# Optimization experiments

Measured on AMD Instinct MI355X. Metric: run time of the kernel, lower is better.

## Reference

```python
import jax, jax.numpy as jnp
import numpy as np

B, N, T, D, H, ET, C = 64, 64, 60, 4, 64, 4, 16
E = N * (N - 1)


def _forward(data, rel_type, rel_rec, rel_send, clinical,
             msg_w1, msg_b1, msg_w2, msg_b2,
             clinh_w1, clinh_b1, clinh_w2, clinh_b2, clinh_w3, clinh_b3,
             clinm_w1, clinm_b1, clinm_w2, clinm_b2, clinm_w3, clinm_b3,
             in_r_w, in_r_b, in_z_w, in_z_b, in_n_w, in_n_b,
             hr_w, hr_b, hn_w, hn_b,
             out1_w, out1_b, out2_w, out2_b, out3_w, out3_b):
    def mlp3(x, w1, b1, w2, b2, w3, b3):
        h1 = jax.nn.relu(x @ w1 + b1)
        h2 = jax.nn.relu(h1 @ w2 + b2)
        return h2 @ w3 + b3

    Bn, Nn, Tn, Dn = data.shape
    ETn = msg_w1.shape[0]
    inputs = jnp.transpose(data, (0, 2, 1, 3))  # [B,T,N,D]
    # cond_hidden: initial hidden from clinical MLP
    hidden = mlp3(clinical, clinh_w1, clinh_b1, clinh_w2, clinh_b2, clinh_w3, clinh_b3).reshape(Bn, Nn, -1)
    # cond_msgs: per-node clinical message embedding (constant across steps)
    cln_msg = mlp3(clinical, clinm_w1, clinm_b1, clinm_w2, clinm_b2, clinm_w3, clinm_b3).reshape(Bn, Nn, -1)

    def step(carry, _):
        x, h = carry  # x: [B,N,D], h: [B,N,H]
        recv = jnp.einsum('ea,bah->beh', rel_rec, h)
        send = jnp.einsum('ea,bah->beh', rel_send, h)
        pre = jnp.concatenate([recv, send], axis=-1)  # [B,E,2H]
        # all edge-type message MLPs batched over type axis t
        m = jnp.tanh(jnp.einsum('bef,tfh->bteh', pre, msg_w1) + msg_b1[None, :, None, :])
        m = jnp.tanh(jnp.einsum('bteh,thg->bteg', m, msg_w2) + msg_b2[None, :, None, :])
        all_msgs = jnp.einsum('bteh,bet->beh', m, rel_type) / ETn  # weight by rel_type, norm = edge_types
        agg = jnp.einsum('ea,beh->bah', rel_rec, all_msgs) / Dn + cln_msg  # [B,N,H]
        hr_a = agg @ hr_w + hr_b
        r = jax.nn.sigmoid(x @ in_r_w + in_r_b + hr_a)
        # NOTE: original code uses self.hr (not self.hz) for the z gate; bug preserved.
        z = jax.nn.sigmoid(x @ in_z_w + in_z_b + hr_a)
        n = jnp.tanh(x @ in_n_w + in_n_b + r * (agg @ hn_w + hn_b))
        h_new = (1.0 - z) * n + z * h
        p = jax.nn.relu(h_new @ out1_w + out1_b)
        p = jax.nn.relu(p @ out2_w + out2_b)
        pred = x + (p @ out3_w + out3_b)
        return (pred, h_new), pred

    x0 = inputs[:, 0]
    _, preds = jax.lax.scan(step, (x0, hidden), None, length=Tn - 1)  # [T-1,B,N,D]
    pred_all = jnp.concatenate([x0[None], preds], axis=0)  # [T,B,N,D]
    return jnp.transpose(pred_all, (1, 2, 0, 3))  # [B,N,T,D]


def setup_inputs() -> dict:
    key = jax.random.key(0)
    ks = jax.random.split(key, 64)
    cnt = [0]

    def nk():
        cnt[0] += 1
        return ks[cnt[0]]

    def p(shape):
        fan = shape[-2] if len(shape) > 1 else shape[0]
        return jax.random.normal(nk(), shape, jnp.float32) / np.sqrt(fan)

    off = ~np.eye(N, dtype=bool)
    eye = np.eye(N, dtype=np.float32)
    rel_rec = jnp.asarray(eye[np.where(off)[0]])   # [E,N] one-hot receivers
    rel_send = jnp.asarray(eye[np.where(off)[1]])  # [E,N] one-hot senders

    inp = {
        'data': jax.random.normal(nk(), (B, N, T, D), jnp.float32),
        'rel_type': jax.nn.softmax(jax.random.normal(nk(), (B, E, ET), jnp.float32), axis=-1),
        'rel_rec': rel_rec,
        'rel_send': rel_send,
        'clinical': jax.random.normal(nk(), (B, C), jnp.float32),
        'msg_w1': p((ET, 2 * H, H)), 'msg_b1': p((ET, H)),
        'msg_w2': p((ET, H, H)), 'msg_b2': p((ET, H)),
        'clinh_w1': p((C, H)), 'clinh_b1': p((H,)),
        'clinh_w2': p((H, 2 * H)), 'clinh_b2': p((2 * H,)),
        'clinh_w3': p((2 * H, N * H)), 'clinh_b3': p((N * H,)),
        'clinm_w1': p((C, H)), 'clinm_b1': p((H,)),
        'clinm_w2': p((H, 2 * H)), 'clinm_b2': p((2 * H,)),
        'clinm_w3': p((2 * H, N * H)), 'clinm_b3': p((N * H,)),
        'in_r_w': p((D, H)), 'in_r_b': p((H,)),
        'in_z_w': p((D, H)), 'in_z_b': p((H,)),
        'in_n_w': p((D, H)), 'in_n_b': p((H,)),
        'hr_w': p((H, H)), 'hr_b': p((H,)),
        'hn_w': p((H, H)), 'hn_b': p((H,)),
        'out1_w': p((H, H)), 'out1_b': p((H,)),
        'out2_w': p((H, H)), 'out2_b': p((H,)),
        'out3_w': p((H, D)), 'out3_b': p((D,)),
    }
    return inp


def reference(data, rel_type, rel_rec, rel_send, clinical,
              msg_w1, msg_b1, msg_w2, msg_b2,
              clinh_w1, clinh_b1, clinh_w2, clinh_b2, clinh_w3, clinh_b3,
              clinm_w1, clinm_b1, clinm_w2, clinm_b2, clinm_w3, clinm_b3,
              in_r_w, in_r_b, in_z_w, in_z_b, in_n_w, in_n_b,
              hr_w, hr_b, hn_w, hn_b,
              out1_w, out1_b, out2_w, out2_b, out3_w, out3_b):
    return _forward(data, rel_type, rel_rec, rel_send, clinical,
                    msg_w1, msg_b1, msg_w2, msg_b2,
                    clinh_w1, clinh_b1, clinh_w2, clinh_b2, clinh_w3, clinh_b3,
                    clinm_w1, clinm_b1, clinm_w2, clinm_b2, clinm_w3, clinm_b3,
                    in_r_w, in_r_b, in_z_w, in_z_b, in_n_w, in_n_b,
                    hr_w, hr_b, hn_w, hn_b,
                    out1_w, out1_b, out2_w, out2_b, out3_w, out3_b)
```

## Files before the change

kernel.cpp:

```cpp
#include <hip/hip_runtime.h>

#define Bz 64
#define Nz 64
#define Tz 60
#define Dz 4
#define Hz 64
#define ETz 4
#define Ez 4032

typedef _Float16 f16x8 __attribute__((ext_vector_type(8)));
typedef float    f32x4 __attribute__((ext_vector_type(4)));
typedef unsigned int u32;
typedef u32      u32x4 __attribute__((ext_vector_type(4)));
typedef unsigned short u16;

__device__ __forceinline__ float ftanh(float x) {
    float e = __expf(2.0f * x);
    return 1.0f - 2.0f * __builtin_amdgcn_rcpf(e + 1.0f);
}
__device__ __forceinline__ float fsig(float x) {
    return __builtin_amdgcn_rcpf(1.0f + __expf(-x));
}
__device__ __forceinline__ u32 pk2(_Float16 a, _Float16 b) {
    u32 ua = (u32)__builtin_bit_cast(u16, a);
    u32 ub = (u32)__builtin_bit_cast(u16, b);
    return ua | (ub << 16);
}

__global__ __launch_bounds__(64) void k_clinical(
    const float* __restrict__ clin,
    const float* __restrict__ hw1, const float* __restrict__ hb1,
    const float* __restrict__ hw2, const float* __restrict__ hb2,
    const float* __restrict__ hw3, const float* __restrict__ hb3,
    const float* __restrict__ mw1, const float* __restrict__ mb1,
    const float* __restrict__ mw2, const float* __restrict__ mb2,
    const float* __restrict__ mw3, const float* __restrict__ mb3,
    float* __restrict__ hidden, float* __restrict__ clnmsg)
{
    int bi = blockIdx.x;
    int b = bi >> 7, head = (bi >> 6) & 1, jb = bi & 63;
    int tid = threadIdx.x;
    const float* w1 = head ? mw1 : hw1; const float* b1 = head ? mb1 : hb1;
    const float* w2 = head ? mw2 : hw2; const float* b2v = head ? mb2 : hb2;
    const float* w3 = head ? mw3 : hw3; const float* b3 = head ? mb3 : hb3;
    float* outp = head ? clnmsg : hidden;

    __shared__ float sc[16], s1[64], s2[128];
    if (tid < 16) sc[tid] = clin[b * 16 + tid];
    __syncthreads();
    {
        float a = b1[tid];
        #pragma unroll
        for (int c = 0; c < 16; ++c) a = fmaf(sc[c], w1[c * 64 + tid], a);
        s1[tid] = fmaxf(a, 0.f);
    }
    __syncthreads();
    #pragma unroll
    for (int hh = 0; hh < 2; ++hh) {
        int jj = hh * 64 + tid;
        float a = b2v[jj];
        #pragma unroll 8
        for (int c = 0; c < 64; ++c) a = fmaf(s1[c], w2[c * 128 + jj], a);
        s2[jj] = fmaxf(a, 0.f);
    }
    __syncthreads();
    {
        int j = jb * 64 + tid;
        float a = b3[j];
        #pragma unroll 8
        for (int c = 0; c < 128; ++c) a = fmaf(s2[c], w3[c * 4096 + j], a);
        outp[b * 4096 + j] = a;
    }
}

__global__ __launch_bounds__(256) void k_wprep(const float* __restrict__ w2,
                                               u16* __restrict__ Whi,
                                               u16* __restrict__ Wlo)
{
    int id = blockIdx.x * 256 + threadIdx.x;
    int j = id & 7, L = (id >> 3) & 63, r = id >> 9;
    int kt = r & 1, n = (r >> 1) & 3, t = r >> 3;
    int k = kt * 32 + ((L >> 4) << 3) + j;
    int g = n * 16 + (L & 15);
    float w = w2[(t * 64 + k) * 64 + g];
    _Float16 h = (_Float16)w;
    _Float16 l = (_Float16)((w - (float)h) * 4096.0f);
    Whi[id] = __builtin_bit_cast(u16, h);
    Wlo[id] = __builtin_bit_cast(u16, l);
}

__global__ __launch_bounds__(256) void k_init(const float* __restrict__ data,
                                              float* __restrict__ xbuf,
                                              float* __restrict__ out)
{
    int i = blockIdx.x * 256 + threadIdx.x;
    int bn = i >> 2, d = i & 3;
    float v = data[bn * (Tz * Dz) + d];
    xbuf[i] = v;
    out[bn * (Tz * Dz) + d] = v;
}

__global__ __launch_bounds__(64) void k_proj2(
    const float* __restrict__ h, const float* __restrict__ w1,
    const float* __restrict__ b1,
    float* __restrict__ Hrb, float* __restrict__ Hs)
{
    int blk = blockIdx.x;
    int b = blk >> 5;
    int n0 = (blk & 31) * 2, n1 = n0 + 1;
    int l = threadIdx.x;
    __shared__ float s0[64], s1v[64];
    s0[l]  = h[(b * 64 + n0) * 64 + l];
    s1v[l] = h[(b * 64 + n1) * 64 + l];
    __syncthreads();
    #pragma unroll 1
    for (int t = 0; t < 4; ++t) {
        const float* w = w1 + t * 8192;
        float bb = b1[t * 64 + l];
        float ar0 = bb, as0 = 0.f, ar1 = bb, as1 = 0.f;
        #pragma unroll 8
        for (int c = 0; c < 64; ++c) {
            float wr = w[c * 64 + l];
            float wsv = w[(c + 64) * 64 + l];
            float h0 = s0[c], h1 = s1v[c];
            ar0 = fmaf(h0, wr, ar0); as0 = fmaf(h0, wsv, as0);
            ar1 = fmaf(h1, wr, ar1); as1 = fmaf(h1, wsv, as1);
        }
        Hrb[((b * 64 + n0) * 4 + t) * 64 + l] = ar0;
        Hrb[((b * 64 + n1) * 4 + t) * 64 + l] = ar1;
        Hs[((b * 4 + t) * 64 + l) * 64 + n0] = as0;
        Hs[((b * 4 + t) * 64 + l) * 64 + n1] = as1;
    }
}

__global__ __launch_bounds__(256, 5) void k_step(
    const float* __restrict__ Hrb, const float* __restrict__ Hs,
    const float* __restrict__ rel_type, const float* __restrict__ b2,
    const u16* __restrict__ Whi, const u16* __restrict__ Wlo,
    const float* __restrict__ cln,
    float* __restrict__ hbuf, float* __restrict__ xbuf,
    const float* __restrict__ irw, const float* __restrict__ irb,
    const float* __restrict__ izw, const float* __restrict__ izb,
    const float* __restrict__ inw, const float* __restrict__ inb,
    const float* __restrict__ hrw, const float* __restrict__ hrbv,
    const float* __restrict__ hnw, const float* __restrict__ hnbv,
    const float* __restrict__ o1w, const float* __restrict__ o1b,
    const float* __restrict__ o2w, const float* __restrict__ o2b,
    const float* __restrict__ o3w, const float* __restrict__ o3b,
    float* __restrict__ out, int tout)
{
    int blk = blockIdx.x;
    int b = blk >> 6, rv = blk & 63;
    int tid = threadIdx.x;
    int w = tid >> 6, L = tid & 63;
    int kg = L >> 4, el = L & 15;
    int e = w * 16 + el;

    __shared__ __align__(16) _Float16 ZaH[4][16][64];
    __shared__ __align__(16) _Float16 ZaL[4][16][64];
    __shared__ __align__(16) float srt[256];
    __shared__ float sRed[4][64];
    __shared__ float sA[64], sH[64], sP[64];

    {
        const float* rbase = rel_type + (b * Ez + rv * 63) * 4;
        float v = (tid < 252) ? rbase[tid] : 0.f;
        srt[(tid & 3) * 64 + (tid >> 2)] = v;
    }
    __syncthreads();

    int snd = (e < 63) ? (e + (e >= rv ? 1 : 0)) : 0;
    int em = el & 7;
    float pacc0 = 0.f, pacc1 = 0.f, pacc2 = 0.f, pacc3 = 0.f;

    #pragma unroll 1
    for (int t = 0; t < 4; ++t) {
        const float* hrp = Hrb + blk * 256 + t * 64 + kg * 16;
        const float* hsp = Hs + (b * 4 + t) * 4096 + kg * 1024 + snd;
        float zv[16];
        #pragma unroll
        for (int j = 0; j < 16; ++j) zv[j] = hrp[j] + hsp[j * 64];
        #pragma unroll
        for (int j = 0; j < 16; ++j) zv[j] = ftanh(zv[j]);

        #pragma unroll
        for (int p = 0; p < 2; ++p) {
            u32 hi[4], lo[4];
            #pragma unroll
            for (int q = 0; q < 4; ++q) {
                float a = zv[p * 8 + 2 * q], c = zv[p * 8 + 2 * q + 1];
                _Float16 ha = (_Float16)a, hc = (_Float16)c;
                _Float16 la = (_Float16)((a - (float)ha) * 4096.0f);
                _Float16 lc = (_Float16)((c - (float)hc) * 4096.0f);
                hi[q] = pk2(ha, hc);
                lo[q] = pk2(la, lc);
            }
            int cp = (2 * kg + p) ^ em;
            u32x4 vh = {hi[0], hi[1], hi[2], hi[3]};
            u32x4 vl = {lo[0], lo[1], lo[2], lo[3]};
            *(u32x4*)&ZaH[w][el][cp * 8] = vh;
            *(u32x4*)&ZaL[w][el][cp * 8] = vl;
        }

        f16x8 Ah[2], Al[2];
        #pragma unroll
        for (int kt = 0; kt < 2; ++kt) {
            int cp = (kt * 4 + kg) ^ em;
            Ah[kt] = *(const f16x8*)&ZaH[w][el][cp * 8];
            Al[kt] = *(const f16x8*)&ZaL[w][el][cp * 8];
        }

        f32x4 rt4 = *(const f32x4*)&srt[t * 64 + w * 16 + kg * 4];

        #pragma unroll
        for (int n = 0; n < 4; ++n) {
            const u16* wb = Whi + ((t * 8 + n * 2) * 64 + L) * 8;
            const u16* wl = Wlo + ((t * 8 + n * 2) * 64 + L) * 8;
            f16x8 Bh0 = *(const f16x8*)wb;
            f16x8 Bh1 = *(const f16x8*)(wb + 512);
            f16x8 Bl0 = *(const f16x8*)wl;
            f16x8 Bl1 = *(const f16x8*)(wl + 512);
            f32x4 hh = {0.f, 0.f, 0.f, 0.f};
            f32x4 cc = {0.f, 0.f, 0.f, 0.f};
            hh = __builtin_amdgcn_mfma_f32_16x16x32_f16(Ah[0], Bh0, hh, 0, 0, 0);
            hh = __builtin_amdgcn_mfma_f32_16x16x32_f16(Ah[1], Bh1, hh, 0, 0, 0);
            cc = __builtin_amdgcn_mfma_f32_16x16x32_f16(Ah[0], Bl0, cc, 0, 0, 0);
            cc = __builtin_amdgcn_mfma_f32_16x16x32_f16(Al[0], Bh0, cc, 0, 0, 0);
            cc = __builtin_amdgcn_mfma_f32_16x16x32_f16(Ah[1], Bl1, cc, 0, 0, 0);
            cc = __builtin_amdgcn_mfma_f32_16x16x32_f16(Al[1], Bh1, cc, 0, 0, 0);
            float b2n = b2[t * 64 + n * 16 + el];
            float acc = 0.f;
            #pragma unroll
            for (int r = 0; r < 4; ++r) {
                float v = fmaf(cc[r], (1.0f / 4096.0f), hh[r]) + b2n;
                acc = fmaf(ftanh(v), rt4[r], acc);
            }
            if (n == 0) pacc0 += acc;
            else if (n == 1) pacc1 += acc;
            else if (n == 2) pacc2 += acc;
            else pacc3 += acc;
        }
    }

    pacc0 += __shfl_xor(pacc0, 16); pacc0 += __shfl_xor(pacc0, 32);
    pacc1 += __shfl_xor(pacc1, 16); pacc1 += __shfl_xor(pacc1, 32);
    pacc2 += __shfl_xor(pacc2, 16); pacc2 += __shfl_xor(pacc2, 32);
    pacc3 += __shfl_xor(pacc3, 16); pacc3 += __shfl_xor(pacc3, 32);
    if (L < 16) {
        sRed[w][0 * 16 + L] = pacc0;
        sRed[w][1 * 16 + L] = pacc1;
        sRed[w][2 * 16 + L] = pacc2;
        sRed[w][3 * 16 + L] = pacc3;
    }
    __syncthreads();
    if (tid < 64) {
        float av = (sRed[0][tid] + sRed[1][tid] + sRed[2][tid] + sRed[3][tid]) * 0.0625f;
        sA[tid] = av + cln[blk * 64 + tid];
    }
    __syncthreads();

    if (w == 0) {
        float h_old = hbuf[blk * 64 + L];
        float x0 = xbuf[blk * 4 + 0], x1 = xbuf[blk * 4 + 1];
        float x2 = xbuf[blk * 4 + 2], x3 = xbuf[blk * 4 + 3];

        float hra = hrbv[L], hna = hnbv[L];
        #pragma unroll 8
        for (int k = 0; k < 64; ++k) {
            float av = sA[k];
            hra = fmaf(av, hrw[k * 64 + L], hra);
            hna = fmaf(av, hnw[k * 64 + L], hna);
        }
        float xr = irb[L], xz = izb[L], xn = inb[L];
        xr = fmaf(x0, irw[L], xr); xr = fmaf(x1, irw[64 + L], xr);
        xr = fmaf(x2, irw[128 + L], xr); xr = fmaf(x3, irw[192 + L], xr);
        xz = fmaf(x0, izw[L], xz); xz = fmaf(x1, izw[64 + L], xz);
        xz = fmaf(x2, izw[128 + L], xz); xz = fmaf(x3, izw[192 + L], xz);
        xn = fmaf(x0, inw[L], xn); xn = fmaf(x1, inw[64 + L], xn);
        xn = fmaf(x2, inw[128 + L], xn); xn = fmaf(x3, inw[192 + L], xn);

        float r = fsig(xr + hra);
        float z = fsig(xz + hra);
        float nn = ftanh(xn + r * hna);
        float hnew = (1.f - z) * nn + z * h_old;
        hbuf[blk * 64 + L] = hnew;
        sH[L] = hnew;

        float p = o1b[L];
        #pragma unroll 8
        for (int k = 0; k < 64; ++k) p = fmaf(sH[k], o1w[k * 64 + L], p);
        p = fmaxf(p, 0.f);
        sP[L] = p;
        float q = o2b[L];
        #pragma unroll 8
        for (int k = 0; k < 64; ++k) q = fmaf(sP[k], o2w[k * 64 + L], q);
        q = fmaxf(q, 0.f);
        sP[L] = q;
        if (L < 4) {
            float xv = (L == 0) ? x0 : (L == 1) ? x1 : (L == 2) ? x2 : x3;
            float pr = xv + o3b[L];
            #pragma unroll 8
            for (int k = 0; k < 64; ++k) pr = fmaf(sP[k], o3w[k * 4 + L], pr);
            out[(blk * Tz + tout) * 4 + L] = pr;
            xbuf[blk * 4 + L] = pr;
        }
    }
}

extern "C" void kernel_launch(void* const* d_in, const int* in_sizes, int n_in,
                              void* d_out, int out_size, void* d_ws, size_t ws_size,
                              hipStream_t stream)
{
    const float* data     = (const float*)d_in[0];
    const float* rel_type = (const float*)d_in[1];
    const float* clinical = (const float*)d_in[4];
    const float* msg_w1 = (const float*)d_in[5];
    const float* msg_b1 = (const float*)d_in[6];
    const float* msg_w2 = (const float*)d_in[7];
    const float* msg_b2 = (const float*)d_in[8];
    const float* chw1 = (const float*)d_in[9];
    const float* chb1 = (const float*)d_in[10];
    const float* chw2 = (const float*)d_in[11];
    const float* chb2 = (const float*)d_in[12];
    const float* chw3 = (const float*)d_in[13];
    const float* chb3 = (const float*)d_in[14];
    const float* cmw1 = (const float*)d_in[15];
    const float* cmb1 = (const float*)d_in[16];
    const float* cmw2 = (const float*)d_in[17];
    const float* cmb2 = (const float*)d_in[18];
    const float* cmw3 = (const float*)d_in[19];
    const float* cmb3 = (const float*)d_in[20];
    const float* irw = (const float*)d_in[21];
    const float* irb = (const float*)d_in[22];
    const float* izw = (const float*)d_in[23];
    const float* izb = (const float*)d_in[24];
    const float* inw = (const float*)d_in[25];
    const float* inb = (const float*)d_in[26];
    const float* hrw = (const float*)d_in[27];
    const float* hrb = (const float*)d_in[28];
    const float* hnw = (const float*)d_in[29];
    const float* hnb = (const float*)d_in[30];
    const float* o1w = (const float*)d_in[31];
    const float* o1b = (const float*)d_in[32];
    const float* o2w = (const float*)d_in[33];
    const float* o2b = (const float*)d_in[34];
    const float* o3w = (const float*)d_in[35];
    const float* o3b = (const float*)d_in[36];

    float* ws   = (float*)d_ws;
    float* hbuf = ws;
    float* cln  = ws + 262144;
    float* Hrb  = ws + 524288;
    float* Hs   = ws + 1572864;
    float* xbuf = ws + 2621440;
    u16*   Whi  = (u16*)(ws + 2637824);
    u16*   Wlo  = (u16*)(ws + 2646016);
    float* out  = (float*)d_out;

    k_clinical<<<dim3(8192), dim3(64), 0, stream>>>(
        clinical, chw1, chb1, chw2, chb2, chw3, chb3,
        cmw1, cmb1, cmw2, cmb2, cmw3, cmb3, hbuf, cln);
    k_wprep<<<dim3(64), dim3(256), 0, stream>>>(msg_w2, Whi, Wlo);
    k_init<<<dim3(64), dim3(256), 0, stream>>>(data, xbuf, out);
    k_proj2<<<dim3(2048), dim3(64), 0, stream>>>(hbuf, msg_w1, msg_b1, Hrb, Hs);

    for (int t = 1; t < Tz; ++t) {
        k_step<<<dim3(Bz * Nz), dim3(256), 0, stream>>>(
            Hrb, Hs, rel_type, msg_b2, Whi, Wlo, cln, hbuf, xbuf,
            irw, irb, izw, izb, inw, inb,
            hrw, hrb, hnw, hnb,
            o1w, o1b, o2w, o2b, o3w, o3b, out, t);
        if (t < Tz - 1)
            k_proj2<<<dim3(2048), dim3(64), 0, stream>>>(hbuf, msg_w1, msg_b1, Hrb, Hs);
    }
}
```

Before: 8.919 ms.

## Remap k_step warps to edge types and process two receiver nodes per block

Each warp now owns one edge type and keeps that type's hi/lo fp16 W2 fragments in registers. Each block handles two receiver nodes and loops over the edge tiles, where before each warp handled a tile of edges and reloaded weights for all four types. Hrb rows and rel_type are staged in shared memory for both nodes, and the grid is halved to 2048 blocks. The aim is to reuse weight loads across more edges, at the cost of higher register pressure (launch bounds lowered to 3) and fewer blocks.

Result: faster. 7.408 ms (-16.9%).

```diff
diff --git a/kernel.cpp b/kernel.cpp
--- a/kernel.cpp
+++ b/kernel.cpp
@@ -133,7 +133,68 @@
     }
 }
 
-__global__ __launch_bounds__(256, 5) void k_step(
+#define RV_TILES(RVS, PACC)                                                    \
+    {                                                                          \
+        const int rv = n0 + (RVS);                                             \
+        _Pragma("unroll 2")                                                    \
+        for (int m = 0; m < 4; ++m) {                                          \
+            int e = m * 16 + el;                                               \
+            int snd = (e < 63) ? (e + (e >= rv ? 1 : 0)) : 0;                  \
+            const float* hs = Hs + (b * 4 + w) * 4096 + kg * 1024 + snd;       \
+            float zv[16];                                                      \
+            _Pragma("unroll")                                                  \
+            for (int j = 0; j < 16; ++j)                                       \
+                zv[j] = sHr[(RVS) * 256 + w * 64 + kg * 16 + j] + hs[j * 64];  \
+            _Pragma("unroll")                                                  \
+            for (int j = 0; j < 16; ++j) zv[j] = ftanh(zv[j]);                 \
+            _Pragma("unroll")                                                  \
+            for (int p = 0; p < 2; ++p) {                                      \
+                u32 hi[4], lo[4];                                              \
+                _Pragma("unroll")                                              \
+                for (int q = 0; q < 4; ++q) {                                  \
+                    float a = zv[p * 8 + 2 * q], c = zv[p * 8 + 2 * q + 1];    \
+                    _Float16 ha = (_Float16)a, hc = (_Float16)c;               \
+                    _Float16 la = (_Float16)((a - (float)ha) * 4096.0f);       \
+                    _Float16 lc = (_Float16)((c - (float)hc) * 4096.0f);       \
+                    hi[q] = pk2(ha, hc);                                       \
+                    lo[q] = pk2(la, lc);                                       \
+                }                                                              \
+                int cp = (2 * kg + p) ^ em;                                    \
+                u32x4 vh = {hi[0], hi[1], hi[2], hi[3]};                       \
+                u32x4 vl = {lo[0], lo[1], lo[2], lo[3]};                       \
+                *(u32x4*)&ZaH[w][el][cp * 8] = vh;                             \
+                *(u32x4*)&ZaL[w][el][cp * 8] = vl;                             \
+            }                                                                  \
+            f16x8 Ah[2], Al[2];                                                \
+            _Pragma("unroll")                                                  \
+            for (int kt = 0; kt < 2; ++kt) {                                   \
+                int cp = (kt * 4 + kg) ^ em;                                   \
+                Ah[kt] = *(const f16x8*)&ZaH[w][el][cp * 8];                   \
+                Al[kt] = *(const f16x8*)&ZaL[w][el][cp * 8];                   \
+            }                                                                  \
+            f32x4 rt4 = *(const f32x4*)&srt[(RVS) * 256 + w * 64 + m * 16 + kg * 4]; \
+            _Pragma("unroll")                                                  \
+            for (int n = 0; n < 4; ++n) {                                      \
+                f32x4 hh = {0.f, 0.f, 0.f, 0.f};                               \
+                f32x4 cc = {0.f, 0.f, 0.f, 0.f};                               \
+                hh = __builtin_amdgcn_mfma_f32_16x16x32_f16(Ah[0], Bh[n*2+0], hh, 0, 0, 0); \
+                hh = __builtin_amdgcn_mfma_f32_16x16x32_f16(Ah[1], Bh[n*2+1], hh, 0, 0, 0); \
+                cc = __builtin_amdgcn_mfma_f32_16x16x32_f16(Ah[0], Bl[n*2+0], cc, 0, 0, 0); \
+                cc = __builtin_amdgcn_mfma_f32_16x16x32_f16(Al[0], Bh[n*2+0], cc, 0, 0, 0); \
+                cc = __builtin_amdgcn_mfma_f32_16x16x32_f16(Ah[1], Bl[n*2+1], cc, 0, 0, 0); \
+                cc = __builtin_amdgcn_mfma_f32_16x16x32_f16(Al[1], Bh[n*2+1], cc, 0, 0, 0); \
+                float acc = 0.f;                                               \
+                _Pragma("unroll")                                              \
+                for (int r = 0; r < 4; ++r) {                                  \
+                    float v = fmaf(cc[r], (1.0f / 4096.0f), hh[r]) + b2n[n];   \
+                    acc = fmaf(ftanh(v), rt4[r], acc);                         \
+                }                                                              \
+                PACC[n] += acc;                                                \
+            }                                                                  \
+        }                                                                      \
+    }
+
+__global__ __launch_bounds__(256, 3) void k_step(
     const float* __restrict__ Hrb, const float* __restrict__ Hs,
     const float* __restrict__ rel_type, const float* __restrict__ b2,
     const u16* __restrict__ Whi, const u16* __restrict__ Wlo,
@@ -150,124 +211,81 @@
     float* __restrict__ out, int tout)
 {
     int blk = blockIdx.x;
-    int b = blk >> 6, rv = blk & 63;
+    int b = blk >> 5;
+    int n0 = (blk & 31) * 2;
     int tid = threadIdx.x;
     int w = tid >> 6, L = tid & 63;
     int kg = L >> 4, el = L & 15;
-    int e = w * 16 + el;
+    int em = el & 7;
 
     __shared__ __align__(16) _Float16 ZaH[4][16][64];
     __shared__ __align__(16) _Float16 ZaL[4][16][64];
-    __shared__ __align__(16) float srt[256];
-    __shared__ float sRed[4][64];
-    __shared__ float sA[64], sH[64], sP[64];
-
-    {
-        const float* rbase = rel_type + (b * Ez + rv * 63) * 4;
-        float v = (tid < 252) ? rbase[tid] : 0.f;
-        srt[(tid & 3) * 64 + (tid >> 2)] = v;
-    }
-    __syncthreads();
-
-    int snd = (e < 63) ? (e + (e >= rv ? 1 : 0)) : 0;
-    int em = el & 7;
-    float pacc0 = 0.f, pacc1 = 0.f, pacc2 = 0.f, pacc3 = 0.f;
-
-    #pragma unroll 1
-    for (int t = 0; t < 4; ++t) {
-        const float* hrp = Hrb + blk * 256 + t * 64 + kg * 16;
-        const float* hsp = Hs + (b * 4 + t) * 4096 + kg * 1024 + snd;
-        float zv[16];
-        #pragma unroll
-        for (int j = 0; j < 16; ++j) zv[j] = hrp[j] + hsp[j * 64];
-        #pragma unroll
-        for (int j = 0; j < 16; ++j) zv[j] = ftanh(zv[j]);
-
-        #pragma unroll
-        for (int p = 0; p < 2; ++p) {
-            u32 hi[4], lo[4];
-            #pragma unroll
-            for (int q = 0; q < 4; ++q) {
-                float a = zv[p * 8 + 2 * q], c = zv[p * 8 + 2 * q + 1];
-                _Float16 ha = (_Float16)a, hc = (_Float16)c;
-                _Float16 la = (_Float16)((a - (float)ha) * 4096.0f);
-                _Float16 lc = (_Float16)((c - (float)hc) * 4096.0f);
-                hi[q] = pk2(ha, hc);
-                lo[q] = pk2(la, lc);
-            }
-            int cp = (2 * kg + p) ^ em;
-            u32x4 vh = {hi[0], hi[1], hi[2], hi[3]};
-            u32x4 vl = {lo[0], lo[1], lo[2], lo[3]};
-            *(u32x4*)&ZaH[w][el][cp * 8] = vh;
-            *(u32x4*)&ZaL[w][el][cp * 8] = vl;
-        }
-
-        f16x8 Ah[2], Al[2];
-        #pragma unroll
-        for (int kt = 0; kt < 2; ++kt) {
-            int cp = (kt * 4 + kg) ^ em;
-            Ah[kt] = *(const f16x8*)&ZaH[w][el][cp * 8];
-            Al[kt] = *(const f16x8*)&ZaL[w][el][cp * 8];
-        }
-
-        f32x4 rt4 = *(const f32x4*)&srt[t * 64 + w * 16 + kg * 4];
-
+    __shared__ __align__(16) float srt[512];
+    __shared__ __align__(16) float sHr[512];
+    __shared__ float sRed[4][2][64];
+    __shared__ float sA[128], sH[128], sP[128];
+
+    #pragma unroll
+    for (int it = 0; it < 2; ++it) {
+        int idx = it * 256 + tid;
+        int rvs = idx >> 8, r = idx & 255;
+        float v = 0.f;
+        if (r < 252) v = rel_type[(b * Ez + (n0 + rvs) * 63) * 4 + r];
+        srt[rvs * 256 + (r & 3) * 64 + (r >> 2)] = v;
+        sHr[idx] = Hrb[(b * 64 + n0) * 256 + idx];
+    }
+    __syncthreads();
+
+    f16x8 Bh[8], Bl[8];
+    #pragma unroll
+    for (int nk = 0; nk < 8; ++nk) {
+        Bh[nk] = *(const f16x8*)(Whi + ((w * 8 + nk) * 64 + L) * 8);
+        Bl[nk] = *(const f16x8*)(Wlo + ((w * 8 + nk) * 64 + L) * 8);
+    }
+    float b2n[4];
+    #pragma unroll
+    for (int n = 0; n < 4; ++n) b2n[n] = b2[w * 64 + n * 16 + el];
+
+    float pA[4] = {0.f, 0.f, 0.f, 0.f};
+    float pB[4] = {0.f, 0.f, 0.f, 0.f};
+    RV_TILES(0, pA)
+    RV_TILES(1, pB)
+
+    #pragma unroll
+    for (int n = 0; n < 4; ++n) {
+        pA[n] += __shfl_xor(pA[n], 16); pA[n] += __shfl_xor(pA[n], 32);
+        pB[n] += __shfl_xor(pB[n], 16); pB[n] += __shfl_xor(pB[n], 32);
+    }
+    if (L < 16) {
         #pragma unroll
         for (int n = 0; n < 4; ++n) {
-            const u16* wb = Whi + ((t * 8 + n * 2) * 64 + L) * 8;
-            const u16* wl = Wlo + ((t * 8 + n * 2) * 64 + L) * 8;
-            f16x8 Bh0 = *(const f16x8*)wb;
-            f16x8 Bh1 = *(const f16x8*)(wb + 512);
-            f16x8 Bl0 = *(const f16x8*)wl;
-            f16x8 Bl1 = *(const f16x8*)(wl + 512);
-            f32x4 hh = {0.f, 0.f, 0.f, 0.f};
-            f32x4 cc = {0.f, 0.f, 0.f, 0.f};
-            hh = __builtin_amdgcn_mfma_f32_16x16x32_f16(Ah[0], Bh0, hh, 0, 0, 0);
-            hh = __builtin_amdgcn_mfma_f32_16x16x32_f16(Ah[1], Bh1, hh, 0, 0, 0);
-            cc = __builtin_amdgcn_mfma_f32_16x16x32_f16(Ah[0], Bl0, cc, 0, 0, 0);
-            cc = __builtin_amdgcn_mfma_f32_16x16x32_f16(Al[0], Bh0, cc, 0, 0, 0);
-            cc = __builtin_amdgcn_mfma_f32_16x16x32_f16(Ah[1], Bl1, cc, 0, 0, 0);
-            cc = __builtin_amdgcn_mfma_f32_16x16x32_f16(Al[1], Bh1, cc, 0, 0, 0);
-            float b2n = b2[t * 64 + n * 16 + el];
-            float acc = 0.f;
-            #pragma unroll
-            for (int r = 0; r < 4; ++r) {
-                float v = fmaf(cc[r], (1.0f / 4096.0f), hh[r]) + b2n;
-                acc = fmaf(ftanh(v), rt4[r], acc);
-            }
-            if (n == 0) pacc0 += acc;
-            else if (n == 1) pacc1 += acc;
-            else if (n == 2) pacc2 += acc;
-            else pacc3 += acc;
+            sRed[w][0][n * 16 + L] = pA[n];
+            sRed[w][1][n * 16 + L] = pB[n];
         }
     }
-
-    pacc0 += __shfl_xor(pacc0, 16); pacc0 += __shfl_xor(pacc0, 32);
-    pacc1 += __shfl_xor(pacc1, 16); pacc1 += __shfl_xor(pacc1, 32);
-    pacc2 += __shfl_xor(pacc2, 16); pacc2 += __shfl_xor(pacc2, 32);
-    pacc3 += __shfl_xor(pacc3, 16); pacc3 += __shfl_xor(pacc3, 32);
-    if (L < 16) {
-        sRed[w][0 * 16 + L] = pacc0;
-        sRed[w][1 * 16 + L] = pacc1;
-        sRed[w][2 * 16 + L] = pacc2;
-        sRed[w][3 * 16 + L] = pacc3;
-    }
-    __syncthreads();
-    if (tid < 64) {
-        float av = (sRed[0][tid] + sRed[1][tid] + sRed[2][tid] + sRed[3][tid]) * 0.0625f;
-        sA[tid] = av + cln[blk * 64 + tid];
-    }
-    __syncthreads();
-
-    if (w == 0) {
-        float h_old = hbuf[blk * 64 + L];
-        float x0 = xbuf[blk * 4 + 0], x1 = xbuf[blk * 4 + 1];
-        float x2 = xbuf[blk * 4 + 2], x3 = xbuf[blk * 4 + 3];
+    __syncthreads();
+    if (tid < 128) {
+        int rvs = tid >> 6, ch = tid & 63;
+        float av = (sRed[0][rvs][ch] + sRed[1][rvs][ch] +
+                    sRed[2][rvs][ch] + sRed[3][rvs][ch]) * 0.0625f;
+        sA[rvs * 64 + ch] = av + cln[(b * 64 + n0 + rvs) * 64 + ch];
+    }
+    __syncthreads();
+
+    if (w < 2) {
+        int node = b * 64 + n0 + w;
+        const float* sAp = sA + w * 64;
+        float* sHp = sH + w * 64;
+        float* sPp = sP + w * 64;
+
+        float h_old = hbuf[node * 64 + L];
+        float x0 = xbuf[node * 4 + 0], x1 = xbuf[node * 4 + 1];
+        float x2 = xbuf[node * 4 + 2], x3 = xbuf[node * 4 + 3];
 
         float hra = hrbv[L], hna = hnbv[L];
         #pragma unroll 8
         for (int k = 0; k < 64; ++k) {
-            float av = sA[k];
+            float av = sAp[k];
             hra = fmaf(av, hrw[k * 64 + L], hra);
             hna = fmaf(av, hnw[k * 64 + L], hna);
         }
@@ -283,26 +301,26 @@
         float z = fsig(xz + hra);
         float nn = ftanh(xn + r * hna);
         float hnew = (1.f - z) * nn + z * h_old;
-        hbuf[blk * 64 + L] = hnew;
-        sH[L] = hnew;
+        hbuf[node * 64 + L] = hnew;
+        sHp[L] = hnew;
 
         float p = o1b[L];
         #pragma unroll 8
-        for (int k = 0; k < 64; ++k) p = fmaf(sH[k], o1w[k * 64 + L], p);
+        for (int k = 0; k < 64; ++k) p = fmaf(sHp[k], o1w[k * 64 + L], p);
         p = fmaxf(p, 0.f);
-        sP[L] = p;
+        sPp[L] = p;
         float q = o2b[L];
         #pragma unroll 8
-        for (int k = 0; k < 64; ++k) q = fmaf(sP[k], o2w[k * 64 + L], q);
+        for (int k = 0; k < 64; ++k) q = fmaf(sPp[k], o2w[k * 64 + L], q);
         q = fmaxf(q, 0.f);
-        sP[L] = q;
+        sPp[L] = q;
         if (L < 4) {
             float xv = (L == 0) ? x0 : (L == 1) ? x1 : (L == 2) ? x2 : x3;
             float pr = xv + o3b[L];
             #pragma unroll 8
-            for (int k = 0; k < 64; ++k) pr = fmaf(sP[k], o3w[k * 4 + L], pr);
-            out[(blk * Tz + tout) * 4 + L] = pr;
-            xbuf[blk * 4 + L] = pr;
+            for (int k = 0; k < 64; ++k) pr = fmaf(sPp[k], o3w[k * 4 + L], pr);
+            out[(node * Tz + tout) * 4 + L] = pr;
+            xbuf[node * 4 + L] = pr;
         }
     }
 }
@@ -365,7 +383,7 @@
     k_proj2<<<dim3(2048), dim3(64), 0, stream>>>(hbuf, msg_w1, msg_b1, Hrb, Hs);
 
     for (int t = 1; t < Tz; ++t) {
-        k_step<<<dim3(Bz * Nz), dim3(256), 0, stream>>>(
+        k_step<<<dim3(2048), dim3(256), 0, stream>>>(
             Hrb, Hs, rel_type, msg_b2, Whi, Wlo, cln, hbuf, xbuf,
             irw, irb, izw, izb, inw, inb,
             hrw, hrb, hnw, hnb,
```
